# Kernel tuning notes

Hardware: AMD Instinct MI355X
Metric: run time of the kernel (lower is better)

The kernel has to match this reference:

```python
import jax, jax.numpy as jnp
import numpy as np

N_RBF = 32
R_CUT = 5.0
LAMBDA = 1.0

# real spherical harmonic constants
_C1 = float(np.sqrt(3.0 / (4.0 * np.pi)))            # l=1
_C2A = float(0.5 * np.sqrt(15.0 / np.pi))            # xy, yz, xz
_C2B = float(0.25 * np.sqrt(5.0 / np.pi))            # 3z^2-1
_C2C = float(0.25 * np.sqrt(15.0 / np.pi))           # x^2-y^2


def _sph_l1_l2(u):
    # u: (P,3) unit vectors -> (P, 3+5) real spherical harmonics for l=1,2
    x, y, z = u[:, 0], u[:, 1], u[:, 2]
    l1 = jnp.stack([_C1 * y, _C1 * z, _C1 * x], axis=-1)
    l2 = jnp.stack([
        _C2A * x * y,
        _C2A * y * z,
        _C2B * (3.0 * z * z - 1.0),
        _C2A * x * z,
        _C2C * (x * x - y * y),
    ], axis=-1)
    return jnp.concatenate([l1, l2], axis=-1)


def setup_inputs() -> dict:
    key = jax.random.key(0)
    k1, k2, k3, k4 = jax.random.split(key, 4)
    n, n_pairs = 100000, 3200000
    R = jax.random.normal(k1, (n, 3), dtype=jnp.float32)
    idx_i = jnp.sort(jax.random.randint(k2, (n_pairs,), 0, n, dtype=jnp.int32))
    idx_j = jax.random.randint(k3, (n_pairs,), 0, n, dtype=jnp.int32)
    z = jax.random.randint(k4, (n,), 0, 100, dtype=jnp.int32)
    pair_mask = jnp.ones((n_pairs,), dtype=jnp.float32)
    point_mask = jnp.ones((n,), dtype=jnp.float32)
    return {"R": R, "pair_mask": pair_mask, "point_mask": point_mask,
            "idx_i": idx_i, "idx_j": idx_j, "z": z}


def reference(R, pair_mask, point_mask, idx_i, idx_j, z):
    # gather + displacement, masked (safe_scale)
    r_ij = (R[idx_j] - R[idx_i]) * pair_mask[:, None]          # (P,3)
    # safe norm (avoid NaN grad at r==0)
    sq = jnp.sum(r_ij * r_ij, axis=-1)
    d_ij = jnp.where(sq == 0, 0.0, jnp.sqrt(jnp.where(sq == 0, 1.0, sq)))
    d_ij = d_ij * pair_mask                                    # (P,)

    # gaussian RBF on equidistant centers in [0, r_cut]
    centers = jnp.linspace(0.0, R_CUT, N_RBF, dtype=jnp.float32)
    width = R_CUT / N_RBF
    rbf_ij = jnp.exp(-0.5 * ((d_ij[:, None] - centers) / width) ** 2)
    rbf_ij = rbf_ij * pair_mask[:, None]                       # (P, n_rbf)

    # cosine cutoff
    phi_r_cut = 0.5 * (jnp.cos(jnp.pi * d_ij / R_CUT) + 1.0)
    phi_r_cut = phi_r_cut * (d_ij < R_CUT).astype(d_ij.dtype) * pair_mask

    # safe unit vector (safe_mask)
    denom = jnp.where(d_ij[:, None] == 0, 1.0, d_ij[:, None])
    unit_r_ij = jnp.where(d_ij[:, None] != 0, r_ij / denom, 0.0)
    unit_r_ij = unit_r_ij * pair_mask[:, None]

    # spherical harmonics for degrees [1,2]
    sph_ij = _sph_l1_l2(unit_r_ij) * pair_mask[:, None]        # (P, 8)

    # SPHC: cutoff-weighted scatter-sum per center atom (bincount over idx_i)
    weighted = sph_ij * phi_r_cut[:, None]                     # (P, 8)
    chi = jax.ops.segment_sum(weighted, idx_i, num_segments=R.shape[0])
    chi = chi * point_mask[:, None] / LAMBDA                   # (n, 8)

    return rbf_ij, chi
```

## Files before the change

kernel.cpp:

```cpp
#include <hip/hip_runtime.h>


#define NRBF 32
constexpr float R_CUT   = 5.0f;
constexpr float WIDTH   = R_CUT / NRBF;
constexpr float INV_W   = 1.0f / WIDTH;
constexpr float CSPACE  = R_CUT / (NRBF - 1);
constexpr float PI_F    = 3.14159265358979323846f;
constexpr float LOG2E   = 1.44269504088896340736f;
constexpr float EXP2_A  = -0.5f * LOG2E * INV_W * INV_W;
constexpr float C1  = 0.48860251190291992f;
constexpr float C2A = 1.09254843059207907f;
constexpr float C2B = 0.31539156525252005f;
constexpr float C2C = 0.54627421529603953f;

#define DPP_ROW_SHR(n)  (0x110 + (n))
#define DPP_ROW_BCAST15 0x142
#define DPP_ROW_BCAST31 0x143

template <int CTRL>
__device__ __forceinline__ float fdpp0(float x) {
    return __int_as_float(__builtin_amdgcn_update_dpp(
        0, __float_as_int(x), CTRL, 0xF, 0xF, true));
}

__global__ __launch_bounds__(256) void geom_pairs_kernel(
    const float* __restrict__ R,
    const float* __restrict__ pair_mask,
    const float* __restrict__ point_mask,
    const int*   __restrict__ idx_i,
    const int*   __restrict__ idx_j,
    float* __restrict__ rbf_out,
    float* __restrict__ chi_out,
    int n_pairs)
{
    const int p    = blockIdx.x * blockDim.x + threadIdx.x;
    const int lane = threadIdx.x & 63;

    int   seg  = -1;
    float d_bc = 1e30f;
    float w[8];
    #pragma unroll
    for (int c = 0; c < 8; ++c) w[c] = 0.0f;

    if (p < n_pairs) {
        const int i = idx_i[p];
        const int j = idx_j[p];
        const float m = pair_mask[p];
        seg = i;

        const float rx = (R[3*j+0] - R[3*i+0]) * m;
        const float ry = (R[3*j+1] - R[3*i+1]) * m;
        const float rz = (R[3*j+2] - R[3*i+2]) * m;

        const float sq = rx*rx + ry*ry + rz*rz;
        const float d  = sqrtf(sq) * m;

        d_bc = (m != 0.0f) ? d : 1e30f;

        float phi = 0.5f * (__cosf(PI_F * d * (1.0f/R_CUT)) + 1.0f);
        phi *= (d < R_CUT) ? 1.0f : 0.0f;
        phi *= m;

        const float inv_d = (d != 0.0f) ? (1.0f / d) : 0.0f;
        const float ux = rx * inv_d * m;
        const float uy = ry * inv_d * m;
        const float uz = rz * inv_d * m;

        float s[8];
        s[0] = C1  * uy;
        s[1] = C1  * uz;
        s[2] = C1  * ux;
        s[3] = C2A * ux * uy;
        s[4] = C2A * uy * uz;
        s[5] = C2B * (3.0f * uz * uz - 1.0f) * m;
        s[6] = C2A * ux * uz;
        s[7] = C2C * (ux * ux - uy * uy);

        const float scale = phi * point_mask[i];
        #pragma unroll
        for (int c = 0; c < 8; ++c) w[c] = s[c] * scale;
    }

    {
        const long long wbase = (long long)(p - lane);
        const int sub = lane & 7;
        const int grp = lane >> 3;
        #pragma unroll
        for (int it = 0; it < 8; ++it) {
            const int srcl = it * 8 + grp;
            const float dd = __shfl(d_bc, srcl, 64);
            const long long pr = wbase + srcl;
            if (pr < (long long)n_pairs) {
                const float base = dd - (float)(4 * sub) * CSPACE;
                const float a0 = base;
                const float a1 = base - CSPACE;
                const float a2 = base - 2.0f * CSPACE;
                const float a3 = base - 3.0f * CSPACE;
                float4 v;
                v.x = __builtin_amdgcn_exp2f(EXP2_A * a0 * a0);
                v.y = __builtin_amdgcn_exp2f(EXP2_A * a1 * a1);
                v.z = __builtin_amdgcn_exp2f(EXP2_A * a2 * a2);
                v.w = __builtin_amdgcn_exp2f(EXP2_A * a3 * a3);
                *(float4*)(rbf_out + pr * NRBF + 4 * sub) = v;
            }
        }
    }

    {
        const int prev_seg = __shfl_up(seg, 1, 64);
        const bool head = (lane == 0) || (prev_seg != seg);
        const unsigned long long H = __ballot(head);
        const unsigned long long below = (2ull << lane) - 1ull;
        const int s = 63 - __clzll(H & below);

        {
            const bool ok = (lane - 1) >= s;
            #pragma unroll
            for (int c = 0; c < 8; ++c) { float t = fdpp0<DPP_ROW_SHR(1)>(w[c]); if (ok) w[c] += t; }
        }
        {
            const bool ok = (lane - 2) >= s;
            #pragma unroll
            for (int c = 0; c < 8; ++c) { float t = fdpp0<DPP_ROW_SHR(2)>(w[c]); if (ok) w[c] += t; }
        }
        {
            const bool ok = (lane - 4) >= s;
            #pragma unroll
            for (int c = 0; c < 8; ++c) { float t = fdpp0<DPP_ROW_SHR(4)>(w[c]); if (ok) w[c] += t; }
        }
        {
            const bool ok = (lane - 8) >= s;
            #pragma unroll
            for (int c = 0; c < 8; ++c) { float t = fdpp0<DPP_ROW_SHR(8)>(w[c]); if (ok) w[c] += t; }
        }
        {
            const bool ok = ((lane >> 4) & 1) && (s < (lane & ~15));
            #pragma unroll
            for (int c = 0; c < 8; ++c) { float t = fdpp0<DPP_ROW_BCAST15>(w[c]); if (ok) w[c] += t; }
        }
        {
            const bool ok = (lane >= 32) && (s < 32);
            #pragma unroll
            for (int c = 0; c < 8; ++c) { float t = fdpp0<DPP_ROW_BCAST31>(w[c]); if (ok) w[c] += t; }
        }

        const bool tail = (lane == 63) || (((H >> 1) >> lane) & 1ull);
        if (tail && seg >= 0) {
            float* dst = chi_out + (size_t)seg * 8;
            #pragma unroll
            for (int c = 0; c < 8; ++c) unsafeAtomicAdd(dst + c, w[c]);
        }
    }
}

extern "C" void kernel_launch(void* const* d_in, const int* in_sizes, int n_in,
                              void* d_out, int out_size, void* d_ws, size_t ws_size,
                              hipStream_t stream) {
    const float* R          = (const float*)d_in[0];
    const float* pair_mask  = (const float*)d_in[1];
    const float* point_mask = (const float*)d_in[2];
    const int*   idx_i      = (const int*)d_in[3];
    const int*   idx_j      = (const int*)d_in[4];

    const int n_pairs = in_sizes[1];
    const int n       = in_sizes[2];

    float* rbf_out = (float*)d_out;
    float* chi_out = rbf_out + (size_t)n_pairs * NRBF;

    hipMemsetAsync(chi_out, 0, (size_t)n * 8 * sizeof(float), stream);

    const int block = 256;
    const int grid  = (n_pairs + block - 1) / block;
    geom_pairs_kernel<<<grid, block, 0, stream>>>(
        R, pair_mask, point_mask, idx_i, idx_j, rbf_out, chi_out, n_pairs);
}
```

Baseline: 488.0 us.

## Pack positions into float4 workspace and use nontemporal loads/stores

Adds a small pre-kernel that repacks R into 16-byte aligned float4 entries in the workspace, so each gather of a position becomes one vector load instead of three scalar loads. Streaming inputs (idx_i, idx_j, pair_mask) and the large RBF output now use nontemporal loads and stores to keep them from polluting cache, leaving more room for the gathered positions. This costs an extra kernel launch and workspace use, and falls back to the old path when no workspace is available.

```diff
diff --git a/kernel.cpp b/kernel.cpp
--- a/kernel.cpp
+++ b/kernel.cpp
@@ -18,18 +18,29 @@
 #define DPP_ROW_BCAST15 0x142
 #define DPP_ROW_BCAST31 0x143
 
+typedef float f32x4 __attribute__((ext_vector_type(4)));
+
 template <int CTRL>
 __device__ __forceinline__ float fdpp0(float x) {
     return __int_as_float(__builtin_amdgcn_update_dpp(
         0, __float_as_int(x), CTRL, 0xF, 0xF, true));
 }
 
+__global__ __launch_bounds__(256) void pack_kernel(
+    const float* __restrict__ R, float4* __restrict__ R4, int n)
+{
+    const int t = blockIdx.x * blockDim.x + threadIdx.x;
+    if (t < n) R4[t] = make_float4(R[3*t+0], R[3*t+1], R[3*t+2], 0.0f);
+}
+
+template <bool PACKED>
 __global__ __launch_bounds__(256) void geom_pairs_kernel(
-    const float* __restrict__ R,
-    const float* __restrict__ pair_mask,
-    const float* __restrict__ point_mask,
-    const int*   __restrict__ idx_i,
-    const int*   __restrict__ idx_j,
+    const float*  __restrict__ R,
+    const float4* __restrict__ R4,
+    const float*  __restrict__ pair_mask,
+    const float*  __restrict__ point_mask,
+    const int*    __restrict__ idx_i,
+    const int*    __restrict__ idx_j,
     float* __restrict__ rbf_out,
     float* __restrict__ chi_out,
     int n_pairs)
@@ -44,14 +55,25 @@
     for (int c = 0; c < 8; ++c) w[c] = 0.0f;
 
     if (p < n_pairs) {
-        const int i = idx_i[p];
-        const int j = idx_j[p];
-        const float m = pair_mask[p];
+        const int   i = __builtin_nontemporal_load(idx_i + p);
+        const int   j = __builtin_nontemporal_load(idx_j + p);
+        const float m = __builtin_nontemporal_load(pair_mask + p);
         seg = i;
 
-        const float rx = (R[3*j+0] - R[3*i+0]) * m;
-        const float ry = (R[3*j+1] - R[3*i+1]) * m;
-        const float rz = (R[3*j+2] - R[3*i+2]) * m;
+        float rjx, rjy, rjz, rix, riy, riz;
+        if (PACKED) {
+            const float4 qj = R4[j];
+            const float4 qi = R4[i];
+            rjx = qj.x; rjy = qj.y; rjz = qj.z;
+            rix = qi.x; riy = qi.y; riz = qi.z;
+        } else {
+            rjx = R[3*j+0]; rjy = R[3*j+1]; rjz = R[3*j+2];
+            rix = R[3*i+0]; riy = R[3*i+1]; riz = R[3*i+2];
+        }
+
+        const float rx = (rjx - rix) * m;
+        const float ry = (rjy - riy) * m;
+        const float rz = (rjz - riz) * m;
 
         const float sq = rx*rx + ry*ry + rz*rz;
         const float d  = sqrtf(sq) * m;
@@ -97,12 +119,13 @@
                 const float a1 = base - CSPACE;
                 const float a2 = base - 2.0f * CSPACE;
                 const float a3 = base - 3.0f * CSPACE;
-                float4 v;
+                f32x4 v;
                 v.x = __builtin_amdgcn_exp2f(EXP2_A * a0 * a0);
                 v.y = __builtin_amdgcn_exp2f(EXP2_A * a1 * a1);
                 v.z = __builtin_amdgcn_exp2f(EXP2_A * a2 * a2);
                 v.w = __builtin_amdgcn_exp2f(EXP2_A * a3 * a3);
-                *(float4*)(rbf_out + pr * NRBF + 4 * sub) = v;
+                __builtin_nontemporal_store(
+                    v, (f32x4*)(rbf_out + pr * NRBF + 4 * sub));
             }
         }
     }
@@ -173,6 +196,15 @@
 
     const int block = 256;
     const int grid  = (n_pairs + block - 1) / block;
-    geom_pairs_kernel<<<grid, block, 0, stream>>>(
-        R, pair_mask, point_mask, idx_i, idx_j, rbf_out, chi_out, n_pairs);
-}
+
+    const bool packed = (d_ws != nullptr) && (ws_size >= (size_t)n * 16);
+    if (packed) {
+        float4* R4 = (float4*)d_ws;
+        pack_kernel<<<(n + block - 1) / block, block, 0, stream>>>(R, R4, n);
+        geom_pairs_kernel<true><<<grid, block, 0, stream>>>(
+            R, R4, pair_mask, point_mask, idx_i, idx_j, rbf_out, chi_out, n_pairs);
+    } else {
+        geom_pairs_kernel<false><<<grid, block, 0, stream>>>(
+            R, nullptr, pair_mask, point_mask, idx_i, idx_j, rbf_out, chi_out, n_pairs);
+    }
+}
```

Result: faster. 478.1 us (-2.0%).
